# Kernel tuning notes

Hardware: AMD Instinct MI355X
Metric: run time of the kernel (lower is better)

Reference implementation:

```python
import jax, jax.numpy as jnp
import numpy as np

D = 256          # feature_dim
H = 4            # num_heads (hard-coded in AdaAttentionalPropagation)
HD = D // H      # per-head dim = 64
L = 6            # number of layers
B, N, M = 2, 2048, 2048
NAMES = ("self", "cross", "self", "cross", "self", "cross")
POOLS = (1, 1, 2, 2, 2, 2)
EPS = 1e-5


def conv1x1(W, b, x):
    # Conv1d kernel_size=1 == pointwise linear over channels: x [B, Cin, N] -> [B, Cout, N]
    return jnp.einsum('oi,bin->bon', W, x) + b[None, :, None]


def inst_norm(x):
    # InstanceNorm1d(affine=False): normalize over spatial dim per (batch, channel)
    mu = jnp.mean(x, axis=-1, keepdims=True)
    var = jnp.var(x, axis=-1, keepdims=True)
    return (x - mu) * jax.lax.rsqrt(var + EPS)


def attn_prop(params, x, source, mask):
    # One AdaAttentionalPropagation layer. x [B,D,Nq], source [B,D,Nk], mask [B,Nq,Nk]
    Wq, bq, Wk, bk, Wv, bv, Wm, bm, W1, b1, W2, b2 = params
    b = x.shape[0]
    q = conv1x1(Wq, bq, x).reshape(b, HD, H, -1)       # [B, hd, H, Nq]
    k = conv1x1(Wk, bk, source).reshape(b, HD, H, -1)  # [B, hd, H, Nk]
    v = conv1x1(Wv, bv, source).reshape(b, HD, H, -1)
    scores = jnp.einsum('bdhn,bdhm->bhnm', q, k) / np.sqrt(HD).astype(np.float32)
    scores = scores * mask[:, None]                     # multiplicative pruned mask
    prob = jax.nn.softmax(scores, axis=-1)              # [B, H, Nq, Nk]
    att = jnp.einsum('bhnm,bdhm->bdhn', prob, v).reshape(b, D, -1)
    message = conv1x1(Wm, bm, att)                      # merge
    y = jnp.concatenate([x, message], axis=1)           # [B, 2D, Nq]
    h = jax.nn.relu(inst_norm(conv1x1(W1, b1, y)))      # MLP_IN hidden
    delta = conv1x1(W2, b2, h)                          # [B, D, Nq]
    return delta, jnp.mean(prob, axis=1)                # prob averaged over heads


def prune(conn, prob, pool, k_cur):
    # update_connections_by_pooling_size: keep top (k_cur // pool) entries per row
    if prob is None or pool == 1:
        return conn, k_cur
    k_new = k_cur // pool
    vals, idxs = jax.lax.top_k(prob, k_new)             # over last axis
    b, n, _ = conn.shape
    new = jnp.zeros_like(conn).at[
        jnp.arange(b)[:, None, None], jnp.arange(n)[None, :, None], idxs
    ].set(jnp.where(vals > 0, 1.0, 0.0).astype(conn.dtype))
    return jax.lax.stop_gradient(new), k_new


def setup_inputs() -> dict:
    key = jax.random.key(0)
    ks = jax.random.split(key, 16)
    s1 = 1.0 / np.sqrt(D)
    s2 = 1.0 / np.sqrt(2 * D)
    return {
        "desc0": jax.random.normal(ks[0], (B, D, N), dtype=jnp.float32),
        "desc1": jax.random.normal(ks[1], (B, D, M), dtype=jnp.float32),
        "Wq": jax.random.normal(ks[2], (L, D, D), dtype=jnp.float32) * s1,
        "bq": jax.random.normal(ks[3], (L, D), dtype=jnp.float32) * 0.01,
        "Wk": jax.random.normal(ks[4], (L, D, D), dtype=jnp.float32) * s1,
        "bk": jax.random.normal(ks[5], (L, D), dtype=jnp.float32) * 0.01,
        "Wv": jax.random.normal(ks[6], (L, D, D), dtype=jnp.float32) * s1,
        "bv": jax.random.normal(ks[7], (L, D), dtype=jnp.float32) * 0.01,
        "Wm": jax.random.normal(ks[8], (L, D, D), dtype=jnp.float32) * s1,
        "bm": jax.random.normal(ks[9], (L, D), dtype=jnp.float32) * 0.01,
        "W1": jax.random.normal(ks[10], (L, 2 * D, 2 * D), dtype=jnp.float32) * s2,
        "b1": jax.random.normal(ks[11], (L, 2 * D), dtype=jnp.float32) * 0.01,
        "W2": jax.random.normal(ks[12], (L, D, 2 * D), dtype=jnp.float32) * s2,
        "b2": jnp.zeros((L, D), dtype=jnp.float32),  # nn.init.constant_(mlp[-1].bias, 0)
    }


def reference(desc0, desc1, Wq, bq, Wk, bk, Wv, bv, Wm, bm, W1, b1, W2, b2):
    b = desc0.shape[0]
    n, m = desc0.shape[2], desc1.shape[2]
    masks = {
        '00': jnp.ones((b, n, n), jnp.float32), '01': jnp.ones((b, n, m), jnp.float32),
        '11': jnp.ones((b, m, m), jnp.float32), '10': jnp.ones((b, m, n), jnp.float32),
    }
    probs = {'00': None, '01': None, '11': None, '10': None}
    kcnt = {'00': n, '01': m, '11': m, '10': n}
    for i in range(L):
        params = (Wq[i], bq[i], Wk[i], bk[i], Wv[i], bv[i],
                  Wm[i], bm[i], W1[i], b1[i], W2[i], b2[i])
        pool = POOLS[i]
        if NAMES[i] == 'cross':
            masks['01'], kcnt['01'] = prune(masks['01'], probs['01'], pool, kcnt['01'])
            delta0, probs['01'] = attn_prop(params, desc0, desc1, masks['01'])
            masks['10'], kcnt['10'] = prune(masks['10'], probs['10'], pool, kcnt['10'])
            delta1, probs['10'] = attn_prop(params, desc1, desc0, masks['10'])
        else:
            masks['00'], kcnt['00'] = prune(masks['00'], probs['00'], pool, kcnt['00'])
            delta0, probs['00'] = attn_prop(params, desc0, desc0, masks['00'])
            masks['11'], kcnt['11'] = prune(masks['11'], probs['11'], pool, kcnt['11'])
            delta1, probs['11'] = attn_prop(params, desc1, desc1, masks['11'])
        desc0 = desc0 + delta0
        desc1 = desc1 + delta1
    return jnp.stack([desc0, desc1])  # [2, B, D, N]
```

## Files before the change

### kernel.cpp

```cpp
#include <hip/hip_runtime.h>
#include <hip/hip_bf16.h>
#include <stdint.h>

#define NPTS 2048
#define MB_ROW 256L
#define MB_B   ((long)NPTS * MB_ROW)
#define MB_T   (2 * MB_B)

typedef __attribute__((ext_vector_type(8))) short bf16x8;
typedef __attribute__((ext_vector_type(4))) float f32x4;
#define MFMA16 __builtin_amdgcn_mfma_f32_16x16x32_bf16

__device__ inline unsigned short f2b(float f) {
  union { float f; unsigned int u; } x; x.f = f;
  unsigned int u = x.u;
  return (unsigned short)((u + 0x7FFFu + ((u >> 16) & 1u)) >> 16);
}
__device__ inline float bfu(unsigned int us) {
  union { unsigned int u; float f; } x; x.u = (us & 0xFFFFu) << 16;
  return x.f;
}
__device__ inline void sp3(float x, unsigned short& h, unsigned short& m, unsigned short& l) {
  h = f2b(x);
  float r1 = x - bfu(h);
  m = f2b(r1);
  l = f2b(r1 - bfu(m));
}
__device__ inline void gld16(const unsigned short* g, unsigned short* l) {
  __builtin_amdgcn_global_load_lds(
      (const __attribute__((address_space(1))) void*)g,
      (__attribute__((address_space(3))) void*)l, 16, 0, 0);
}

#define E_P3  0
#define E_V3  1
#define E_S3  2
#define E_Y3  3
#define E_H   4
#define E_RES 5

template <int EPI>
__global__ __launch_bounds__(256) void t3_k(
    const unsigned short* __restrict__ A, long aps,
    const unsigned short* __restrict__ B, long bps,
    const unsigned short* __restrict__ B2, long b2ps,
    const float* __restrict__ bias,
    void* __restrict__ out,
    const unsigned char* __restrict__ masks,
    int K, int lda, int ldb, int ksplit, long sps,
    int zbase, int xorv, int selfl, int yoff) {
  const int t = threadIdx.x;
  const int z = blockIdx.z;
  const int zg = zbase + z;
  long aoff = 0, boff = 0, b2off = 0;
  if constexpr (EPI == E_P3 || EPI == E_V3) {
    boff = (long)z * 524288;
  } else if constexpr (EPI == E_S3) {
    const int sb = zg >> 2, h = zg & 3;
    aoff = (long)zg * 131072;
    boff = (long)((sb ^ xorv) * 4 + h) * 131072;
  } else if constexpr (EPI == E_Y3) {
    boff = (long)zg * 524288;
  } else if constexpr (EPI == E_H) {
    boff = (long)zg * 524288;
    b2off = (long)z * 524288;
  } else {
    boff = (long)z * 1048576;
  }
  const int n0 = blockIdx.x * 64;
  const int m0 = ((EPI == E_S3) ? yoff : 0) + blockIdx.y * 64;

  __shared__ __align__(16) unsigned short As[3][64 * 64];
  __shared__ __align__(16) unsigned short Bs[3][64 * 64];
  __shared__ unsigned int Ms[128];
  if constexpr (EPI == E_S3) {
    if (t < 128) {
      const int sb = zg >> 2;
      const int type = selfl ? (sb >> 1) : 2 + (sb >> 1);
      const unsigned int* mw =
          (const unsigned int*)(masks + (long)type * MB_T + (long)(sb & 1) * MB_B);
      Ms[t] = mw[(long)(m0 + (t >> 1)) * 64 + (n0 >> 5) + (t & 1)];
    }
  }

  const int w = t >> 6;
  const int L = t & 63;
  const int wm = (w & 1) * 32, wn = (w >> 1) * 32;
  const int lr = t & 15, lk = (t >> 4) & 3;
  const int swr = (lr & 7) << 3;
  const int grow = (L >> 3);
  const int gj = L & 7;

  f32x4 acc[2][2];
#pragma unroll
  for (int i = 0; i < 2; ++i)
#pragma unroll
    for (int j = 0; j < 2; ++j) acc[i][j] = (f32x4){0.f, 0.f, 0.f, 0.f};

  for (int k0 = 0; k0 < K; k0 += 64) {
    const unsigned short* Bsel;
    long bo, bp;
    int kb;
    if (k0 < ksplit) { Bsel = B; bo = boff; bp = bps; kb = k0; }
    else             { Bsel = B2; bo = b2off; bp = b2ps; kb = k0 - ksplit; }
    if (k0) __syncthreads();
#pragma unroll
    for (int pl = 0; pl < 3; ++pl) {
      const unsigned short* Ap = A + (long)pl * aps + aoff;
      const unsigned short* Bp = Bsel + (long)pl * bp + bo;
#pragma unroll
      for (int c = 0; c < 2; ++c) {
        const int rbase = w * 16 + c * 8;
        const int row = rbase + grow;
        const int colA = (gj ^ (row & 7)) << 3;
        gld16(&Ap[(long)(m0 + row) * lda + k0 + colA], &As[pl][rbase * 64]);
        gld16(&Bp[(long)(n0 + row) * ldb + kb + colA], &Bs[pl][rbase * 64]);
      }
    }
    __syncthreads();
#pragma unroll
    for (int kk = 0; kk < 2; ++kk) {
      bf16x8 af[3][2], bf[3][2];
#pragma unroll
      for (int pl = 0; pl < 3; ++pl)
#pragma unroll
        for (int mi = 0; mi < 2; ++mi) {
          af[pl][mi] = *(const bf16x8*)&As[pl][(wm + mi * 16 + lr) * 64 + ((kk * 32 + lk * 8) ^ swr)];
          bf[pl][mi] = *(const bf16x8*)&Bs[pl][(wn + mi * 16 + lr) * 64 + ((kk * 32 + lk * 8) ^ swr)];
        }
#pragma unroll
      for (int mi = 0; mi < 2; ++mi)
#pragma unroll
        for (int ni = 0; ni < 2; ++ni) {
          f32x4 c = acc[mi][ni];
          c = MFMA16(af[2][mi], bf[0][ni], c, 0, 0, 0);
          c = MFMA16(af[0][mi], bf[2][ni], c, 0, 0, 0);
          c = MFMA16(af[1][mi], bf[1][ni], c, 0, 0, 0);
          c = MFMA16(af[1][mi], bf[0][ni], c, 0, 0, 0);
          c = MFMA16(af[0][mi], bf[1][ni], c, 0, 0, 0);
          c = MFMA16(af[0][mi], bf[0][ni], c, 0, 0, 0);
          acc[mi][ni] = c;
        }
    }
  }

  if constexpr (EPI == E_S3) {
    __syncthreads();
    float* ST = (float*)&As[0][0];
#pragma unroll
    for (int mi = 0; mi < 2; ++mi)
#pragma unroll
      for (int ni = 0; ni < 2; ++ni)
#pragma unroll
        for (int r = 0; r < 4; ++r)
          ST[(wm + mi * 16 + lk * 4 + r) * 68 + wn + ni * 16 + lr] = acc[mi][ni][r];
    __syncthreads();
    float* o = (float*)out;
#pragma unroll
    for (int it = 0; it < 4; ++it) {
      const int row = (t >> 4) + it * 16;
      const int col = (t & 15) * 4;
      float4 vv = *(const float4*)&ST[row * 68 + col];
      const unsigned int mw = Ms[row * 2 + (col >> 5)];
      vv.x = ((mw >> ((col + 0) & 31)) & 1u) ? vv.x * 0.125f : 0.f;
      vv.y = ((mw >> ((col + 1) & 31)) & 1u) ? vv.y * 0.125f : 0.f;
      vv.z = ((mw >> ((col + 2) & 31)) & 1u) ? vv.z * 0.125f : 0.f;
      vv.w = ((mw >> ((col + 3) & 31)) & 1u) ? vv.w * 0.125f : 0.f;
      const int rloc = blockIdx.y * 64 + row;
      *(float4*)&o[(long)z * sps + (long)rloc * 2048 + n0 + col] = vv;
    }
    return;
  }

#pragma unroll
  for (int mi = 0; mi < 2; ++mi) {
#pragma unroll
    for (int ni = 0; ni < 2; ++ni) {
      f32x4 a = acc[mi][ni];
      const int cM = m0 + wm + mi * 16 + lk * 4;
      const int pN = n0 + wn + ni * 16 + lr;
      if constexpr (EPI == E_P3) {
        float4 bv4 = *(const float4*)&bias[cM];
        float bb[4] = {bv4.x, bv4.y, bv4.z, bv4.w};
        unsigned short* o = (unsigned short*)out;
        const long b0 = (long)z * 524288 + (long)pN * 64 + (cM >> 2);
#pragma unroll
        for (int r = 0; r < 4; ++r) {
          unsigned short h_, m_, l_;
          sp3(a[r] + bb[r], h_, m_, l_);
          const long ad = b0 + (long)r * 131072;
          o[ad] = h_; o[ad + 2097152] = m_; o[ad + 4194304] = l_;
        }
      } else if constexpr (EPI == E_V3) {
        float4 bv4 = *(const float4*)&bias[cM];
        float bb[4] = {bv4.x, bv4.y, bv4.z, bv4.w};
        unsigned short* o = (unsigned short*)out;
        const long b0 = (long)z * 524288 + (long)(cM >> 2) * 2048 + pN;
#pragma unroll
        for (int r = 0; r < 4; ++r) {
          unsigned short h_, m_, l_;
          sp3(a[r] + bb[r], h_, m_, l_);
          const long ad = b0 + (long)r * 131072;
          o[ad] = h_; o[ad + 2097152] = m_; o[ad + 4194304] = l_;
        }
      } else if constexpr (EPI == E_Y3) {
        float4 bv4 = *(const float4*)&bias[cM];
        float bb[4] = {bv4.x, bv4.y, bv4.z, bv4.w};
        unsigned short* o = (unsigned short*)out;
        ushort4 h4, m4, l4;
        unsigned short* hp = (unsigned short*)&h4;
        unsigned short* mp = (unsigned short*)&m4;
        unsigned short* lp = (unsigned short*)&l4;
#pragma unroll
        for (int r = 0; r < 4; ++r) sp3(a[r] + bb[r], hp[r], mp[r], lp[r]);
        const long b0 = (long)z * 524288 + (long)pN * 256 + cM;
        *(ushort4*)&o[b0] = h4;
        *(ushort4*)&o[b0 + sps] = m4;
        *(ushort4*)&o[b0 + 2 * sps] = l4;
      } else if constexpr (EPI == E_H) {
        *(f32x4*)&((float*)out)[(long)z * 1048576 + (long)pN * 512 + cM] = a;
      } else {
        float4 bv4 = *(const float4*)&bias[cM];
        float* p = &((float*)out)[(long)zg * 524288 + (long)pN * 256 + cM];
        float4 old = *(const float4*)p;
        float4 nw;
        nw.x = old.x + a[0] + bv4.x; nw.y = old.y + a[1] + bv4.y;
        nw.z = old.z + a[2] + bv4.z; nw.w = old.w + a[3] + bv4.w;
        *(float4*)p = nw;
      }
    }
  }
}

__global__ __launch_bounds__(256) void pv3_k(
    const unsigned short* __restrict__ V3, const float* __restrict__ S, long sps,
    const float2* __restrict__ stats, int CH,
    float* __restrict__ part, int zbase, int xorv) {
  const int t = threadIdx.x;
  const int h = blockIdx.z;
  const int kseg = blockIdx.y;
  const int n0 = blockIdx.x * 64;
  const int sb = zbase >> 2;
  const unsigned short* Vb = V3 + (long)((sb ^ xorv) * 4 + h) * 131072;
  const float* Sp = S + (long)h * sps;
  const float2* sth = stats + (long)h * CH;

  __shared__ __align__(16) unsigned short Bs[3][64 * 64];

  const int w = t >> 6;
  const int wm = (w & 1) * 32, wn = (w >> 1) * 32;
  const int lr = t & 15, lk = (t >> 4) & 3;
  const int srow = t >> 3, scol = (t & 7) * 8;
  const int sws = scol ^ ((srow & 7) << 3);
  const int swr = (lr & 7) << 3;

  f32x4 acc[2][2];
#pragma unroll
  for (int i = 0; i < 2; ++i)
#pragma unroll
    for (int j = 0; j < 2; ++j) acc[i][j] = (f32x4){0.f, 0.f, 0.f, 0.f};

  const int kbeg = kseg * 256;
  const float2 st0 = sth[n0 + srow];
  const float2 st1 = sth[n0 + 32 + srow];
  const float* srcA = &Sp[(long)(n0 + srow) * 2048 + kbeg + scol];
  const float* srcB = &Sp[(long)(n0 + 32 + srow) * 2048 + kbeg + scol];

  float4 c0a = *(const float4*)srcA;
  float4 c0b = *(const float4*)(srcA + 4);
  float4 c1a = *(const float4*)srcB;
  float4 c1b = *(const float4*)(srcB + 4);

#pragma unroll
  for (int ki = 0; ki < 4; ++ki) {
    const int k0 = kbeg + ki * 64;
    float4 n0a, n0b, n1a, n1b;
    if (ki < 3) {
      const int off = (ki + 1) * 64;
      n0a = *(const float4*)(srcA + off);
      n0b = *(const float4*)(srcA + off + 4);
      n1a = *(const float4*)(srcB + off);
      n1b = *(const float4*)(srcB + off + 4);
    }
    if (ki) __syncthreads();
    {
      float xs[8] = {c0a.x, c0a.y, c0a.z, c0a.w, c0b.x, c0b.y, c0b.z, c0b.w};
      ushort4 hq[2], mq[2], lq[2];
      unsigned short* hp = (unsigned short*)hq;
      unsigned short* mp = (unsigned short*)mq;
      unsigned short* lp = (unsigned short*)lq;
#pragma unroll
      for (int j = 0; j < 8; ++j) {
        float p = __expf(xs[j] - st0.x) * st0.y;
        sp3(p, hp[j], mp[j], lp[j]);
      }
      *(ushort4*)&Bs[0][srow * 64 + sws] = hq[0];
      *(ushort4*)&Bs[0][srow * 64 + sws + 4] = hq[1];
      *(ushort4*)&Bs[1][srow * 64 + sws] = mq[0];
      *(ushort4*)&Bs[1][srow * 64 + sws + 4] = mq[1];
      *(ushort4*)&Bs[2][srow * 64 + sws] = lq[0];
      *(ushort4*)&Bs[2][srow * 64 + sws + 4] = lq[1];
    }
    {
      float xs[8] = {c1a.x, c1a.y, c1a.z, c1a.w, c1b.x, c1b.y, c1b.z, c1b.w};
      ushort4 hq[2], mq[2], lq[2];
      unsigned short* hp = (unsigned short*)hq;
      unsigned short* mp = (unsigned short*)mq;
      unsigned short* lp = (unsigned short*)lq;
#pragma unroll
      for (int j = 0; j < 8; ++j) {
        float p = __expf(xs[j] - st1.x) * st1.y;
        sp3(p, hp[j], mp[j], lp[j]);
      }
      const int rr = 32 + srow;
      *(ushort4*)&Bs[0][rr * 64 + sws] = hq[0];
      *(ushort4*)&Bs[0][rr * 64 + sws + 4] = hq[1];
      *(ushort4*)&Bs[1][rr * 64 + sws] = mq[0];
      *(ushort4*)&Bs[1][rr * 64 + sws + 4] = mq[1];
      *(ushort4*)&Bs[2][rr * 64 + sws] = lq[0];
      *(ushort4*)&Bs[2][rr * 64 + sws + 4] = lq[1];
    }
    __syncthreads();
#pragma unroll
    for (int kk = 0; kk < 2; ++kk) {
      bf16x8 af[3][2], bf[3][2];
#pragma unroll
      for (int pl = 0; pl < 3; ++pl) {
#pragma unroll
        for (int mi = 0; mi < 2; ++mi) {
          af[pl][mi] = *(const bf16x8*)&Vb[(long)pl * 2097152 +
                                           (long)(wm + mi * 16 + lr) * 2048 + k0 + kk * 32 + lk * 8];
          bf[pl][mi] = *(const bf16x8*)&Bs[pl][(wn + mi * 16 + lr) * 64 + ((kk * 32 + lk * 8) ^ swr)];
        }
      }
#pragma unroll
      for (int mi = 0; mi < 2; ++mi)
#pragma unroll
        for (int ni = 0; ni < 2; ++ni) {
          f32x4 c = acc[mi][ni];
          c = MFMA16(af[2][mi], bf[0][ni], c, 0, 0, 0);
          c = MFMA16(af[0][mi], bf[2][ni], c, 0, 0, 0);
          c = MFMA16(af[1][mi], bf[1][ni], c, 0, 0, 0);
          c = MFMA16(af[1][mi], bf[0][ni], c, 0, 0, 0);
          c = MFMA16(af[0][mi], bf[1][ni], c, 0, 0, 0);
          c = MFMA16(af[0][mi], bf[0][ni], c, 0, 0, 0);
          acc[mi][ni] = c;
        }
    }
    if (ki < 3) { c0a = n0a; c0b = n0b; c1a = n1a; c1b = n1b; }
  }

  float* pp = part + (((long)kseg * 4 + h) * CH) * 64;
#pragma unroll
  for (int mi = 0; mi < 2; ++mi) {
#pragma unroll
    for (int ni = 0; ni < 2; ++ni) {
      const int cM = wm + mi * 16 + lk * 4;
      const int pN = n0 + wn + ni * 16 + lr;
      *(f32x4*)&pp[(long)pN * 64 + cM] = acc[mi][ni];
    }
  }
}

__global__ __launch_bounds__(256) void comb_k(const float* __restrict__ part,
                                              unsigned short* __restrict__ att3,
                                              int CH, int sb, int cb) {
  const int q = threadIdx.x & 63;
  const int g = threadIdx.x >> 6;
  const int nl = blockIdx.x * 4 + g;
  float s[4] = {0.f, 0.f, 0.f, 0.f};
#pragma unroll
  for (int ks = 0; ks < 8; ++ks)
#pragma unroll
    for (int h = 0; h < 4; ++h)
      s[h] += part[(((long)ks * 4 + h) * CH + nl) * 64 + q];
  ushort4 h4, m4, l4;
  unsigned short* hp = (unsigned short*)&h4;
  unsigned short* mp = (unsigned short*)&m4;
  unsigned short* lp = (unsigned short*)&l4;
#pragma unroll
  for (int h = 0; h < 4; ++h) sp3(s[h], hp[h], mp[h], lp[h]);
  const long base = (long)sb * 524288 + (long)(cb + nl) * 256 + 4 * q;
  *(ushort4*)&att3[base] = h4;
  *(ushort4*)&att3[base + 2097152] = m4;
  *(ushort4*)&att3[base + 4194304] = l4;
}

template <int PRUNE>
__global__ __launch_bounds__(256) void softmax_prune_k(
    const float* __restrict__ S, float2* __restrict__ stats,
    unsigned char* __restrict__ masks,
    int knew, int sbG, int cb, int selfl, long sps, int CH) {
  const int t = threadIdx.x;
  const int nl = blockIdx.x;
  const int wv = t >> 6;
  const int lane = t & 63;
  __shared__ float red[2][16];

  float v[4][8];
#pragma unroll
  for (int hh = 0; hh < 4; ++hh) {
    const float* row = S + (long)hh * sps + (long)nl * 2048 + t * 8;
    float4 u0 = *(const float4*)row;
    float4 u1 = *(const float4*)(row + 4);
    v[hh][0] = u0.x; v[hh][1] = u0.y; v[hh][2] = u0.z; v[hh][3] = u0.w;
    v[hh][4] = u1.x; v[hh][5] = u1.y; v[hh][6] = u1.z; v[hh][7] = u1.w;
  }

  float mx[4];
#pragma unroll
  for (int hh = 0; hh < 4; ++hh) {
    float m = v[hh][0];
#pragma unroll
    for (int j = 1; j < 8; ++j) m = fmaxf(m, v[hh][j]);
    for (int o = 32; o; o >>= 1) m = fmaxf(m, __shfl_xor(m, o));
    mx[hh] = m;
  }
  if (lane == 0) {
#pragma unroll
    for (int hh = 0; hh < 4; ++hh) red[0][hh * 4 + wv] = mx[hh];
  }
  __syncthreads();
#pragma unroll
  for (int hh = 0; hh < 4; ++hh)
    mx[hh] = fmaxf(fmaxf(red[0][hh * 4], red[0][hh * 4 + 1]),
                   fmaxf(red[0][hh * 4 + 2], red[0][hh * 4 + 3]));

#pragma unroll
  for (int hh = 0; hh < 4; ++hh)
#pragma unroll
    for (int j = 0; j < 8; ++j) v[hh][j] = __expf(v[hh][j] - mx[hh]);

  float sm[4];
#pragma unroll
  for (int hh = 0; hh < 4; ++hh) {
    float s = 0.f;
#pragma unroll
    for (int j = 0; j < 8; ++j) s += v[hh][j];
    for (int o = 32; o; o >>= 1) s += __shfl_xor(s, o);
    sm[hh] = s;
  }
  if (lane == 0) {
#pragma unroll
    for (int hh = 0; hh < 4; ++hh) red[1][hh * 4 + wv] = sm[hh];
  }
  __syncthreads();
  float ri[4];
#pragma unroll
  for (int hh = 0; hh < 4; ++hh) {
    const float s = red[1][hh * 4] + red[1][hh * 4 + 1] + red[1][hh * 4 + 2] + red[1][hh * 4 + 3];
    ri[hh] = 1.0f / s;
  }
  if (t == 0) {
#pragma unroll
    for (int hh = 0; hh < 4; ++hh)
      stats[(long)hh * CH + nl] = make_float2(mx[hh], ri[hh]);
  }

  if constexpr (PRUNE) {
    float mean[8] = {};
#pragma unroll
    for (int hh = 0; hh < 4; ++hh)
#pragma unroll
      for (int j = 0; j < 8; ++j) mean[j] += 0.25f * (v[hh][j] * ri[hh]);

    __shared__ unsigned int keys[8][256];
    __shared__ int hist[256];
    __shared__ int wred[4];
    __shared__ int sbx[2];
#pragma unroll
    for (int j = 0; j < 8; ++j) keys[j][t] = __float_as_uint(mean[j]);
    unsigned int pref = 0;
    int kneed = knew;
    for (int pass = 0; pass < 4; ++pass) {
      const int shift = 24 - pass * 8;
      hist[t] = 0;
      __syncthreads();
      const unsigned int hm = (pass == 0) ? 0u : (0xFFFFFFFFu << (shift + 8));
#pragma unroll
      for (int j = 0; j < 8; ++j) {
        unsigned int key = keys[j][t];
        if ((key & hm) == pref) atomicAdd(&hist[(key >> shift) & 255], 1);
      }
      __syncthreads();
      const int h = hist[t];
      int s = h;
#pragma unroll
      for (int o = 1; o < 64; o <<= 1) {
        int tmp = __shfl_down(s, o);
        if (lane + o < 64) s += tmp;
      }
      if (lane == 0) wred[wv] = s;
      __syncthreads();
      int addhi = 0;
#pragma unroll
      for (int w2 = 0; w2 < 4; ++w2)
        if (w2 > wv) addhi += wred[w2];
      s += addhi;
      const int above = s - h;
      if (s >= kneed && above < kneed) { sbx[0] = t; sbx[1] = above; }
      __syncthreads();
      pref |= ((unsigned int)sbx[0]) << shift;
      kneed -= sbx[1];
      __syncthreads();
    }
    const unsigned int T = pref;
    const int take = kneed;
    int cnt = 0;
#pragma unroll
    for (int j = 0; j < 8; ++j) cnt += (keys[j][t] == T);
    int pc = cnt;
#pragma unroll
    for (int o = 1; o < 64; o <<= 1) {
      int tmp = __shfl_up(pc, o);
      if (lane >= o) pc += tmp;
    }
    if (lane == 63) wred[wv] = pc;
    __syncthreads();
    int woff = 0;
#pragma unroll
    for (int w2 = 0; w2 < 4; ++w2)
      if (w2 < wv) woff += wred[w2];
    int base = woff + pc - cnt;
    unsigned int byte = 0;
#pragma unroll
    for (int j = 0; j < 8; ++j) {
      unsigned int key = keys[j][t];
      int sel = 0;
      if (key > T) sel = 1;
      else if (key == T) { if (T > 0u && base < take) sel = 1; base++; }
      byte |= (unsigned int)sel << j;
    }
    const int type = selfl ? (sbG >> 1) : 2 + (sbG >> 1);
    unsigned char* mb = masks + (long)type * MB_T + (long)(sbG & 1) * MB_B;
    mb[(long)(cb + nl) * MB_ROW + t] = (unsigned char)byte;
  }
}

__global__ __launch_bounds__(256) void inormA_k(const float* __restrict__ H,
                                                float* __restrict__ partial) {
  const int seg = blockIdx.x, sbl = blockIdx.y;
  const float* hp = H + (long)sbl * 1048576;
  const int t = threadIdx.x;
  float s0 = 0.f, q0 = 0.f, s1 = 0.f, q1 = 0.f;
  const int r0 = seg * 64;
  for (int r = r0; r < r0 + 64; ++r) {
    float x0 = hp[(long)r * 512 + t];
    float x1 = hp[(long)r * 512 + t + 256];
    s0 += x0; q0 = fmaf(x0, x0, q0);
    s1 += x1; q1 = fmaf(x1, x1, q1);
  }
  float* pp = partial + ((long)sbl * 32 + seg) * 1024;
  pp[t] = s0; pp[t + 256] = s1;
  pp[512 + t] = q0; pp[512 + t + 256] = q1;
}

__global__ __launch_bounds__(256) void inormB_k(const float* __restrict__ partial,
                                                float* __restrict__ stats2) {
  const int sbl = blockIdx.x;
  const int t = threadIdx.x;
  const float* pp = partial + (long)sbl * 32768;
  float a0 = 0.f, b0 = 0.f, a1 = 0.f, b1 = 0.f;
  for (int seg = 0; seg < 32; ++seg) {
    const float* p = pp + seg * 1024;
    a0 += p[t]; a1 += p[t + 256];
    b0 += p[512 + t]; b1 += p[512 + t + 256];
  }
  float mu0 = a0 * (1.f / 2048.f);
  float mu1 = a1 * (1.f / 2048.f);
  float rs0 = rsqrtf(b0 * (1.f / 2048.f) - mu0 * mu0 + 1e-5f);
  float rs1 = rsqrtf(b1 * (1.f / 2048.f) - mu1 * mu1 + 1e-5f);
  float* st = stats2 + (long)sbl * 1024;
  st[t] = mu0; st[t + 256] = mu1;
  st[512 + t] = rs0; st[512 + t + 256] = rs1;
}

__global__ __launch_bounds__(256) void inormC_k(const float* __restrict__ H,
                                                const float* __restrict__ stats2,
                                                unsigned short* __restrict__ HB,
                                                long hps) {
  const int seg = blockIdx.x, sbl = blockIdx.y;
  const float* hp = H + (long)sbl * 1048576;
  unsigned short* hb = HB + (long)sbl * 1048576;
  const float* st = stats2 + (long)sbl * 1024;
  const int t = threadIdx.x;
  const float mu0 = st[t], mu1 = st[t + 256];
  const float rs0 = st[512 + t], rs1 = st[512 + t + 256];
  const int r0 = seg * 64;
  for (int r = r0; r < r0 + 64; ++r) {
    float x0 = hp[(long)r * 512 + t];
    float x1 = hp[(long)r * 512 + t + 256];
    float o0 = (x0 - mu0) * rs0; o0 = o0 > 0.f ? o0 : 0.f;
    float o1 = (x1 - mu1) * rs1; o1 = o1 > 0.f ? o1 : 0.f;
    unsigned short h_, m_, l_;
    sp3(o0, h_, m_, l_);
    const long ad0 = (long)r * 512 + t;
    hb[ad0] = h_; hb[ad0 + hps] = m_; hb[ad0 + 2 * hps] = l_;
    sp3(o1, h_, m_, l_);
    const long ad1 = ad0 + 256;
    hb[ad1] = h_; hb[ad1 + hps] = m_; hb[ad1 + 2 * hps] = l_;
  }
}

__global__ __launch_bounds__(256) void split6_k(
    const float* __restrict__ q, const float* __restrict__ k,
    const float* __restrict__ v, const float* __restrict__ m,
    const float* __restrict__ w1, const float* __restrict__ w2,
    unsigned short* __restrict__ dst) {
  long i = ((long)blockIdx.x * 256 + threadIdx.x) * 4;
  const float* src;
  long off, base, ps;
  if (i < 262144) {
    int sel = (int)(i >> 16);
    src = sel == 0 ? q : sel == 1 ? k : sel == 2 ? v : m;
    off = i & 65535; base = (long)sel * 196608; ps = 65536;
  } else if (i < 524288) {
    src = w1; off = i - 262144; base = 786432; ps = 262144;
  } else {
    src = w2; off = i - 524288; base = 1572864; ps = 131072;
  }
  float4 vv = *(const float4*)&src[off];
  float xs[4] = {vv.x, vv.y, vv.z, vv.w};
  ushort4 h4, m4, l4;
  unsigned short* hp = (unsigned short*)&h4;
  unsigned short* mp = (unsigned short*)&m4;
  unsigned short* lp = (unsigned short*)&l4;
#pragma unroll
  for (int j = 0; j < 4; ++j) sp3(xs[j], hp[j], mp[j], lp[j]);
  *(ushort4*)&dst[base + off] = h4;
  *(ushort4*)&dst[base + ps + off] = m4;
  *(ushort4*)&dst[base + 2 * ps + off] = l4;
}

__global__ __launch_bounds__(256) void split3_k(const float* __restrict__ src,
                                                unsigned short* __restrict__ dst,
                                                long plane, long n) {
  long i = ((long)blockIdx.x * 256 + threadIdx.x) * 4;
  if (i >= n) return;
  float4 v = *(const float4*)&src[i];
  float xs[4] = {v.x, v.y, v.z, v.w};
  ushort4 h4, m4, l4;
  unsigned short* hp = (unsigned short*)&h4;
  unsigned short* mp = (unsigned short*)&m4;
  unsigned short* lp = (unsigned short*)&l4;
#pragma unroll
  for (int j = 0; j < 4; ++j) sp3(xs[j], hp[j], mp[j], lp[j]);
  *(ushort4*)&dst[i] = h4;
  *(ushort4*)&dst[plane + i] = m4;
  *(ushort4*)&dst[2 * plane + i] = l4;
}

__global__ __launch_bounds__(256) void tin_k(const float* __restrict__ d0,
                                             const float* __restrict__ d1,
                                             float* __restrict__ descT) {
  __shared__ float tl[32][33];
  const int sb = blockIdx.z, s = sb >> 1, b = sb & 1;
  const float* src = (s ? d1 : d0) + (long)b * 524288;
  const int p0 = blockIdx.x * 32, c0 = blockIdx.y * 32;
  const int tx = threadIdx.x & 31, ty = threadIdx.x >> 5;
#pragma unroll
  for (int i = 0; i < 4; ++i)
    tl[ty + i * 8][tx] = src[(long)(c0 + ty + i * 8) * 2048 + p0 + tx];
  __syncthreads();
#pragma unroll
  for (int i = 0; i < 4; ++i)
    descT[(long)sb * 524288 + (long)(p0 + ty + i * 8) * 256 + c0 + tx] = tl[tx][ty + i * 8];
}

__global__ __launch_bounds__(256) void tout_k(const float* __restrict__ descT,
                                              float* __restrict__ out) {
  __shared__ float tl[32][33];
  const int sb = blockIdx.z;
  const int p0 = blockIdx.x * 32, c0 = blockIdx.y * 32;
  const int tx = threadIdx.x & 31, ty = threadIdx.x >> 5;
#pragma unroll
  for (int i = 0; i < 4; ++i)
    tl[ty + i * 8][tx] = descT[(long)sb * 524288 + (long)(p0 + ty + i * 8) * 256 + c0 + tx];
  __syncthreads();
#pragma unroll
  for (int i = 0; i < 4; ++i)
    out[(long)sb * 524288 + (long)(c0 + ty + i * 8) * 2048 + p0 + tx] = tl[tx][ty + i * 8];
}

extern "C" void kernel_launch(void* const* d_in, const int* in_sizes, int n_in,
                              void* d_out, int out_size, void* d_ws, size_t ws_size,
                              hipStream_t stream) {
  (void)in_sizes; (void)n_in; (void)out_size;
  const float* in_d0 = (const float*)d_in[0];
  const float* in_d1 = (const float*)d_in[1];
  const float* Wq = (const float*)d_in[2];
  const float* bq = (const float*)d_in[3];
  const float* Wk = (const float*)d_in[4];
  const float* bk = (const float*)d_in[5];
  const float* Wv = (const float*)d_in[6];
  const float* bv = (const float*)d_in[7];
  const float* Wm = (const float*)d_in[8];
  const float* bm = (const float*)d_in[9];
  const float* W1 = (const float*)d_in[10];
  const float* b1 = (const float*)d_in[11];
  const float* W2 = (const float*)d_in[12];
  const float* b2 = (const float*)d_in[13];
  (void)b1;

  const long region_b = (long)ws_size - 79429632;
  const int CH = (region_b >= 40992L * 2048) ? 2048
               : (region_b >= 40992L * 1024) ? 1024 : 512;
  const int nchunks = 2048 / CH;
  const long sps = (long)CH * 2048;
  const int mb = (region_b >= 4 * 13766656L) ? 4 : (region_b >= 2 * 13766656L) ? 2 : 1;

  uint8_t* w = (uint8_t*)d_ws;
  float* descT          = (float*)w;
  unsigned short* desc3 = (unsigned short*)(w + 8388608);
  unsigned short* Q3    = (unsigned short*)(w + 20971520);
  unsigned short* K3    = (unsigned short*)(w + 33554432);
  unsigned short* V3    = (unsigned short*)(w + 46137344);
  unsigned short* att3  = (unsigned short*)(w + 58720256);
  unsigned short* wbuf  = (unsigned short*)(w + 71303168);
  unsigned char* masks  = w + 75235328;
  uint8_t* region       = w + 79429632;
  float* S              = (float*)region;
  float* part           = (float*)(region + (long)CH * 32768);
  float2* stats         = (float2*)(region + (long)CH * 32768 + (long)CH * 8192);
  unsigned short* msg3  = (unsigned short*)region;
  float* hbuf           = (float*)(region + (long)mb * 3145728);
  unsigned short* hB3   = (unsigned short*)(region + (long)mb * 7340032);
  float* inpart         = (float*)(region + (long)mb * 13631488);
  float* instats        = (float*)(region + (long)mb * 13631488 + (long)mb * 131072);

  const unsigned short* wq3 = wbuf;
  const unsigned short* wk3 = wbuf + 196608;
  const unsigned short* wv3 = wbuf + 393216;
  const unsigned short* wm3 = wbuf + 589824;
  const unsigned short* w13 = wbuf + 786432;
  const unsigned short* w23 = wbuf + 1572864;

  tin_k<<<dim3(64, 8, 4), 256, 0, stream>>>(in_d0, in_d1, descT);
  hipMemsetAsync(masks, 0xFF, 4 * MB_T, stream);

  for (int l = 0; l < 6; ++l) {
    const int selfl = (l % 2 == 0);
    const int xorv = selfl ? 0 : 2;
    const int knew = (l < 2) ? 1024 : (l < 4) ? 512 : 0;

    split6_k<<<dim3(640), 256, 0, stream>>>(Wq + (long)l * 65536, Wk + (long)l * 65536,
                                            Wv + (long)l * 65536, Wm + (long)l * 65536,
                                            W1 + (long)l * 262144, W2 + (long)l * 131072,
                                            wbuf);
    split3_k<<<dim3(2048), 256, 0, stream>>>(descT, desc3, 2097152, 2097152);

    t3_k<E_P3><<<dim3(32, 4, 4), 256, 0, stream>>>(
        wq3, 65536, desc3, 2097152, nullptr, 0, bq + l * 256, Q3, nullptr,
        256, 256, 256, 1 << 30, 0, 0, 0, 0, 0);
    t3_k<E_P3><<<dim3(32, 4, 4), 256, 0, stream>>>(
        wk3, 65536, desc3, 2097152, nullptr, 0, bk + l * 256, K3, nullptr,
        256, 256, 256, 1 << 30, 0, 0, 0, 0, 0);
    t3_k<E_V3><<<dim3(32, 4, 4), 256, 0, stream>>>(
        wv3, 65536, desc3, 2097152, nullptr, 0, bv + l * 256, V3, nullptr,
        256, 256, 256, 1 << 30, 0, 0, 0, 0, 0);

    for (int sb = 0; sb < 4; ++sb) {
      for (int c = 0; c < nchunks; ++c) {
        const int cb = c * CH;
        t3_k<E_S3><<<dim3(32, CH / 64, 4), 256, 0, stream>>>(
            Q3, 2097152, K3, 2097152, nullptr, 0, nullptr, S, masks,
            64, 64, 64, 1 << 30, sps, sb * 4, xorv, selfl, cb);
        if (knew)
          softmax_prune_k<1><<<dim3(CH), 256, 0, stream>>>(S, stats, masks, knew, sb, cb, selfl, sps, CH);
        else
          softmax_prune_k<0><<<dim3(CH), 256, 0, stream>>>(S, stats, masks, knew, sb, cb, selfl, sps, CH);
        pv3_k<<<dim3(CH / 64, 8, 4), 256, 0, stream>>>(V3, S, sps, stats, CH, part, sb * 4, xorv);
        comb_k<<<dim3(CH / 4), 256, 0, stream>>>(part, att3, CH, sb, cb);
      }
    }

    for (int p = 0; p < 4; p += mb) {
      t3_k<E_Y3><<<dim3(32, 4, mb), 256, 0, stream>>>(
          wm3, 65536, att3, 2097152, nullptr, 0, bm + l * 256, msg3, nullptr,
          256, 256, 256, 1 << 30, (long)mb * 524288, p, 0, 0, 0);
      t3_k<E_H><<<dim3(32, 8, mb), 256, 0, stream>>>(
          w13, 262144, desc3, 2097152, msg3, (long)mb * 524288, nullptr, hbuf, nullptr,
          512, 512, 256, 256, 0, p, 0, 0, 0);
      inormA_k<<<dim3(32, mb), 256, 0, stream>>>(hbuf, inpart);
      inormB_k<<<dim3(mb), 256, 0, stream>>>(inpart, instats);
      inormC_k<<<dim3(32, mb), 256, 0, stream>>>(hbuf, instats, hB3, (long)mb * 1048576);
      t3_k<E_RES><<<dim3(32, 4, mb), 256, 0, stream>>>(
          w23, 131072, hB3, (long)mb * 1048576, nullptr, 0, b2 + l * 256, descT, nullptr,
          512, 512, 512, 1 << 30, 0, p, 0, 0, 0);
    }
  }

  tout_k<<<dim3(64, 8, 4), 256, 0, stream>>>(descT, (float*)d_out);
}
```

Before: 2.902 ms.

## Process one softmax/prune row per wavefront instead of per block

The softmax and top-k prune kernel now assigns each attention row to a single 64-lane wavefront holding 32 values per lane, so a block covers four rows. Row max/sum reductions and the radix-select scan run with wave shuffles only, removing the cross-wave shared-memory reductions and most block barriers. Histograms are kept per wave in shared memory, and mask bytes are written as uchar4. This raises register pressure (32 keys plus a 32-entry mean per lane) and may reduce occupancy. Some __syncthreads remain around the per-wave histograms.

```diff
diff --git a/kernel.cpp b/kernel.cpp
--- a/kernel.cpp
+++ b/kernel.cpp
@@ -391,149 +391,117 @@
     const float* __restrict__ S, float2* __restrict__ stats,
     unsigned char* __restrict__ masks,
     int knew, int sbG, int cb, int selfl, long sps, int CH) {
-  const int t = threadIdx.x;
-  const int nl = blockIdx.x;
-  const int wv = t >> 6;
-  const int lane = t & 63;
-  __shared__ float red[2][16];
-
-  float v[4][8];
+  const int lane = threadIdx.x & 63;
+  const int wv = threadIdx.x >> 6;
+  const int nl = blockIdx.x * 4 + wv;
+
+  float mean[32];
+#pragma unroll
+  for (int j = 0; j < 32; ++j) mean[j] = 0.f;
+
+  float mx4[4], ri4[4];
 #pragma unroll
   for (int hh = 0; hh < 4; ++hh) {
-    const float* row = S + (long)hh * sps + (long)nl * 2048 + t * 8;
-    float4 u0 = *(const float4*)row;
-    float4 u1 = *(const float4*)(row + 4);
-    v[hh][0] = u0.x; v[hh][1] = u0.y; v[hh][2] = u0.z; v[hh][3] = u0.w;
-    v[hh][4] = u1.x; v[hh][5] = u1.y; v[hh][6] = u1.z; v[hh][7] = u1.w;
-  }
-
-  float mx[4];
-#pragma unroll
-  for (int hh = 0; hh < 4; ++hh) {
-    float m = v[hh][0];
-#pragma unroll
-    for (int j = 1; j < 8; ++j) m = fmaxf(m, v[hh][j]);
+    const float* row = S + (long)hh * sps + (long)nl * 2048 + lane * 32;
+    float xs[32];
+#pragma unroll
+    for (int e = 0; e < 8; ++e) {
+      float4 u = *(const float4*)(row + e * 4);
+      xs[e * 4 + 0] = u.x; xs[e * 4 + 1] = u.y;
+      xs[e * 4 + 2] = u.z; xs[e * 4 + 3] = u.w;
+    }
+    float m = xs[0];
+#pragma unroll
+    for (int j = 1; j < 32; ++j) m = fmaxf(m, xs[j]);
     for (int o = 32; o; o >>= 1) m = fmaxf(m, __shfl_xor(m, o));
-    mx[hh] = m;
+    float s = 0.f;
+#pragma unroll
+    for (int j = 0; j < 32; ++j) { xs[j] = __expf(xs[j] - m); s += xs[j]; }
+    for (int o = 32; o; o >>= 1) s += __shfl_xor(s, o);
+    const float ri = 1.0f / s;
+    mx4[hh] = m; ri4[hh] = ri;
+    if (PRUNE) {
+#pragma unroll
+      for (int j = 0; j < 32; ++j) mean[j] += 0.25f * (xs[j] * ri);
+    }
   }
   if (lane == 0) {
 #pragma unroll
-    for (int hh = 0; hh < 4; ++hh) red[0][hh * 4 + wv] = mx[hh];
-  }
-  __syncthreads();
-#pragma unroll
-  for (int hh = 0; hh < 4; ++hh)
-    mx[hh] = fmaxf(fmaxf(red[0][hh * 4], red[0][hh * 4 + 1]),
-                   fmaxf(red[0][hh * 4 + 2], red[0][hh * 4 + 3]));
-
-#pragma unroll
-  for (int hh = 0; hh < 4; ++hh)
-#pragma unroll
-    for (int j = 0; j < 8; ++j) v[hh][j] = __expf(v[hh][j] - mx[hh]);
-
-  float sm[4];
-#pragma unroll
-  for (int hh = 0; hh < 4; ++hh) {
-    float s = 0.f;
-#pragma unroll
-    for (int j = 0; j < 8; ++j) s += v[hh][j];
-    for (int o = 32; o; o >>= 1) s += __shfl_xor(s, o);
-    sm[hh] = s;
-  }
-  if (lane == 0) {
-#pragma unroll
-    for (int hh = 0; hh < 4; ++hh) red[1][hh * 4 + wv] = sm[hh];
-  }
-  __syncthreads();
-  float ri[4];
-#pragma unroll
-  for (int hh = 0; hh < 4; ++hh) {
-    const float s = red[1][hh * 4] + red[1][hh * 4 + 1] + red[1][hh * 4 + 2] + red[1][hh * 4 + 3];
-    ri[hh] = 1.0f / s;
-  }
-  if (t == 0) {
-#pragma unroll
     for (int hh = 0; hh < 4; ++hh)
-      stats[(long)hh * CH + nl] = make_float2(mx[hh], ri[hh]);
+      stats[(long)hh * CH + nl] = make_float2(mx4[hh], ri4[hh]);
   }
 
   if constexpr (PRUNE) {
-    float mean[8] = {};
-#pragma unroll
-    for (int hh = 0; hh < 4; ++hh)
-#pragma unroll
-      for (int j = 0; j < 8; ++j) mean[j] += 0.25f * (v[hh][j] * ri[hh]);
-
-    __shared__ unsigned int keys[8][256];
-    __shared__ int hist[256];
-    __shared__ int wred[4];
-    __shared__ int sbx[2];
-#pragma unroll
-    for (int j = 0; j < 8; ++j) keys[j][t] = __float_as_uint(mean[j]);
+    unsigned int key[32];
+#pragma unroll
+    for (int j = 0; j < 32; ++j) key[j] = __float_as_uint(mean[j]);
+
+    __shared__ int hist[4][256];
+    int* hw = hist[wv];
     unsigned int pref = 0;
     int kneed = knew;
     for (int pass = 0; pass < 4; ++pass) {
       const int shift = 24 - pass * 8;
-      hist[t] = 0;
+      const unsigned int hm = (pass == 0) ? 0u : (0xFFFFFFFFu << (shift + 8));
+#pragma unroll
+      for (int b = 0; b < 4; ++b) hw[lane * 4 + b] = 0;
       __syncthreads();
-      const unsigned int hm = (pass == 0) ? 0u : (0xFFFFFFFFu << (shift + 8));
-#pragma unroll
-      for (int j = 0; j < 8; ++j) {
-        unsigned int key = keys[j][t];
-        if ((key & hm) == pref) atomicAdd(&hist[(key >> shift) & 255], 1);
-      }
+#pragma unroll
+      for (int j = 0; j < 32; ++j)
+        if ((key[j] & hm) == pref) atomicAdd(&hw[(key[j] >> shift) & 255], 1);
       __syncthreads();
-      const int h = hist[t];
-      int s = h;
-#pragma unroll
+      int own[4];
+      int tot = 0;
+#pragma unroll
+      for (int e = 0; e < 4; ++e) { own[e] = hw[lane * 4 + e]; tot += own[e]; }
+      int suf = tot;
       for (int o = 1; o < 64; o <<= 1) {
-        int tmp = __shfl_down(s, o);
-        if (lane + o < 64) s += tmp;
-      }
-      if (lane == 0) wred[wv] = s;
-      __syncthreads();
-      int addhi = 0;
-#pragma unroll
-      for (int w2 = 0; w2 < 4; ++w2)
-        if (w2 > wv) addhi += wred[w2];
-      s += addhi;
-      const int above = s - h;
-      if (s >= kneed && above < kneed) { sbx[0] = t; sbx[1] = above; }
-      __syncthreads();
-      pref |= ((unsigned int)sbx[0]) << shift;
-      kneed -= sbx[1];
-      __syncthreads();
+        int tmp = __shfl_down(suf, o);
+        if (lane + o < 64) suf += tmp;
+      }
+      int run = suf - tot;
+      int pack = 0;
+#pragma unroll
+      for (int e = 3; e >= 0; --e) {
+        const int Sb = run + own[e];
+        if (Sb >= kneed && run < kneed) pack = ((lane * 4 + e) << 20) | (run + 1);
+        run = Sb;
+      }
+      for (int o = 1; o < 64; o <<= 1) pack |= __shfl_xor(pack, o);
+      const int bin = pack >> 20;
+      const int above = (pack & 0xFFFFF) - 1;
+      pref |= ((unsigned int)bin) << shift;
+      kneed -= above;
     }
     const unsigned int T = pref;
     const int take = kneed;
     int cnt = 0;
 #pragma unroll
-    for (int j = 0; j < 8; ++j) cnt += (keys[j][t] == T);
+    for (int j = 0; j < 32; ++j) cnt += (key[j] == T);
     int pc = cnt;
-#pragma unroll
     for (int o = 1; o < 64; o <<= 1) {
       int tmp = __shfl_up(pc, o);
       if (lane >= o) pc += tmp;
     }
-    if (lane == 63) wred[wv] = pc;
-    __syncthreads();
-    int woff = 0;
-#pragma unroll
-    for (int w2 = 0; w2 < 4; ++w2)
-      if (w2 < wv) woff += wred[w2];
-    int base = woff + pc - cnt;
-    unsigned int byte = 0;
-#pragma unroll
-    for (int j = 0; j < 8; ++j) {
-      unsigned int key = keys[j][t];
-      int sel = 0;
-      if (key > T) sel = 1;
-      else if (key == T) { if (T > 0u && base < take) sel = 1; base++; }
-      byte |= (unsigned int)sel << j;
+    int base = pc - cnt;
+    uchar4 ob;
+    unsigned char* obp = (unsigned char*)&ob;
+#pragma unroll
+    for (int byte = 0; byte < 4; ++byte) {
+      unsigned int bb = 0;
+#pragma unroll
+      for (int e = 0; e < 8; ++e) {
+        const int j = byte * 8 + e;
+        int sel = 0;
+        if (key[j] > T) sel = 1;
+        else if (key[j] == T) { if (T > 0u && base < take) sel = 1; base++; }
+        bb |= (unsigned int)sel << e;
+      }
+      obp[byte] = (unsigned char)bb;
     }
     const int type = selfl ? (sbG >> 1) : 2 + (sbG >> 1);
     unsigned char* mb = masks + (long)type * MB_T + (long)(sbG & 1) * MB_B;
-    mb[(long)(cb + nl) * MB_ROW + t] = (unsigned char)byte;
+    *(uchar4*)&mb[(long)(cb + nl) * MB_ROW + lane * 4] = ob;
   }
 }
 
@@ -766,9 +734,9 @@
             Q3, 2097152, K3, 2097152, nullptr, 0, nullptr, S, masks,
             64, 64, 64, 1 << 30, sps, sb * 4, xorv, selfl, cb);
         if (knew)
-          softmax_prune_k<1><<<dim3(CH), 256, 0, stream>>>(S, stats, masks, knew, sb, cb, selfl, sps, CH);
+          softmax_prune_k<1><<<dim3(CH / 4), 256, 0, stream>>>(S, stats, masks, knew, sb, cb, selfl, sps, CH);
         else
-          softmax_prune_k<0><<<dim3(CH), 256, 0, stream>>>(S, stats, masks, knew, sb, cb, selfl, sps, CH);
+          softmax_prune_k<0><<<dim3(CH / 4), 256, 0, stream>>>(S, stats, masks, knew, sb, cb, selfl, sps, CH);
         pv3_k<<<dim3(CH / 64, 8, 4), 256, 0, stream>>>(V3, S, sps, stats, CH, part, sb * 4, xorv);
         comb_k<<<dim3(CH / 4), 256, 0, stream>>>(part, att3, CH, sb, cb);
       }
```

Measured after the change: 2.907 ms. About the same (+0.2%).
